# Kernel optimization log

Measured on AMD Instinct MI355X. Metric: run time of the kernel, lower is better.

The kernel has to match this reference:

```python
import jax, jax.numpy as jnp
import numpy as np

H = 12        # num_heads
HD = 64       # head_dim
D = H * HD    # hidden_size = 768
N = 4096      # number of patches (64x64 grid)
SCALE = HD ** -0.5


def _rotate_half(x):
    half = x.shape[-1] // 2
    x1, x2 = x[..., :half], x[..., half:]
    return jnp.concatenate([-x2, x1], axis=-1)


def setup_inputs() -> dict:
    key = jax.random.key(0)
    ks = jax.random.split(key, 7)
    return {
        "hidden_states": jax.random.normal(ks[0], (N, D), jnp.float32),
        "cos": jax.random.uniform(ks[1], (N, HD), jnp.float32),
        "sin": jax.random.uniform(ks[2], (N, HD), jnp.float32),
        "qkv_w": jax.random.normal(ks[3], (D, 3 * D), jnp.float32) * (D ** -0.5),
        "qkv_b": jax.random.normal(ks[4], (3 * D,), jnp.float32) * 0.02,
        "proj_w": jax.random.normal(ks[5], (D, D), jnp.float32) * (D ** -0.5),
        "proj_b": jax.random.normal(ks[6], (D,), jnp.float32) * 0.02,
    }


def reference(hidden_states, cos, sin, qkv_w, qkv_b, proj_w, proj_b):
    n = hidden_states.shape[0]
    # fused QKV projection: (N, 3D) -> (N, 3, H, HD)
    qkv = (hidden_states @ qkv_w + qkv_b).reshape(n, 3, H, HD)
    q, k, v = qkv[:, 0], qkv[:, 1], qkv[:, 2]  # each (N, H, HD)

    # 2-D RoPE (HF apply_rotary_pos_emb_vision): cos/sin broadcast over heads
    c = cos[:, None, :]
    s = sin[:, None, :]
    q = q * c + _rotate_half(q) * s
    k = k * c + _rotate_half(k) * s

    # full bidirectional attention, heads-first layout
    q = q.transpose(1, 0, 2) * SCALE  # (H, N, HD)
    k = k.transpose(1, 0, 2)
    v = v.transpose(1, 0, 2)
    attn = jnp.einsum('hnd,hmd->hnm', q, k)      # (H, N, N)
    attn = jax.nn.softmax(attn, axis=-1)
    out = jnp.einsum('hnm,hmd->hnd', attn, v)    # (H, N, HD)
    out = out.transpose(1, 0, 2).reshape(n, D)
    return out @ proj_w + proj_b
```

## Files before the change

kernel.cpp:

```cpp
#include <hip/hip_runtime.h>
#include <stdint.h>

#define NTOK 4096
#define NH 12
#define HDIM 64
#define DMODEL 768
#define D3 2304

typedef __attribute__((ext_vector_type(8))) __bf16 bf16x8;
typedef __attribute__((ext_vector_type(4))) float f32x4;
typedef __attribute__((ext_vector_type(4))) unsigned int u32x4;

#define MFMA(a, b, c) __builtin_amdgcn_mfma_f32_16x16x32_bf16((a), (b), (c), 0, 0, 0)

__device__ __forceinline__ uint16_t f2bf(float f) {
  uint32_t u = __builtin_bit_cast(uint32_t, f) + 0x8000u;
  return (uint16_t)(u >> 16);
}
__device__ __forceinline__ uint32_t packrd(float a, float b) {
  uint32_t ua = __builtin_bit_cast(uint32_t, a) + 0x8000u;
  uint32_t ub = __builtin_bit_cast(uint32_t, b) + 0x8000u;
  return __builtin_amdgcn_perm(ub, ua, 0x07060302u);
}
__device__ __forceinline__ uint32_t packtr(float a, float b) {
  return __builtin_amdgcn_perm(__builtin_bit_cast(uint32_t, b), __builtin_bit_cast(uint32_t, a),
                               0x07060302u);
}
__device__ __forceinline__ float bf2f(uint16_t u) {
  uint32_t v = ((uint32_t)u) << 16;
  return __builtin_bit_cast(float, v);
}
__device__ __forceinline__ void gld_lds16(const uint16_t* g, uint16_t* l) {
  __builtin_amdgcn_global_load_lds((const __attribute__((address_space(1))) void*)g,
                                   (__attribute__((address_space(3))) void*)l, 16, 0, 0);
}

__global__ void va_cast_bf16(const float* __restrict__ in, uint16_t* __restrict__ out, int n4) {
  int i = blockIdx.x * 256 + threadIdx.x;
  if (i >= n4) return;
  float4 v = ((const float4*)in)[i];
  ((uint2*)out)[i] = make_uint2(packrd(v.x, v.y), packrd(v.z, v.w));
}

__global__ void va_transpose_cast(const float* __restrict__ W, uint16_t* __restrict__ Wt,
                                  int K, int Ncols) {
  __shared__ uint16_t tile[32][36];
  const int t = threadIdx.x;
  const int k0 = blockIdx.y * 32, n0 = blockIdx.x * 32;
  {
    int i = t >> 3, j = (t & 7) * 4;
    float4 v = *(const float4*)(W + (size_t)(k0 + i) * Ncols + n0 + j);
    tile[i][j + 0] = f2bf(v.x);
    tile[i][j + 1] = f2bf(v.y);
    tile[i][j + 2] = f2bf(v.z);
    tile[i][j + 3] = f2bf(v.w);
  }
  __syncthreads();
  {
    int c = t >> 3, kk = (t & 7) * 4;
    uint32_t lo = (uint32_t)tile[kk + 0][c] | ((uint32_t)tile[kk + 1][c] << 16);
    uint32_t hi = (uint32_t)tile[kk + 2][c] | ((uint32_t)tile[kk + 3][c] << 16);
    *(uint2*)(Wt + (size_t)(n0 + c) * K + k0 + kk) = make_uint2(lo, hi);
  }
}

__global__ __launch_bounds__(256) void va_gemm_qkv(const uint16_t* __restrict__ A,
                                                   const uint16_t* __restrict__ Bt,
                                                   const float* __restrict__ bias,
                                                   const float* __restrict__ cosb,
                                                   const float* __restrict__ sinb,
                                                   uint16_t* __restrict__ Qg,
                                                   uint16_t* __restrict__ Kg,
                                                   uint16_t* __restrict__ Vtg) {
  __shared__ uint16_t As[128 * 32];
  __shared__ uint16_t Bs[128 * 32];
  const int t = threadIdx.x;
  const int w = t >> 6, ln = t & 63, quad = ln >> 4, l15 = ln & 15;
  const int m0 = blockIdx.y * 128, n0 = blockIdx.x * 128;
  const int wm = (w & 1) * 64, wn = (w >> 1) * 64;
  const int srow = t >> 2, scol = (t & 3) * 8;
  f32x4 acc[4][4] = {};
  for (int kk = 0; kk < DMODEL; kk += 32) {
#pragma unroll
    for (int p = 0; p < 2; ++p) {
      gld_lds16(A + (size_t)(m0 + p * 64 + srow) * DMODEL + kk + scol,
                As + (p * 64 + w * 16) * 32);
      gld_lds16(Bt + (size_t)(n0 + p * 64 + srow) * DMODEL + kk + scol,
                Bs + (p * 64 + w * 16) * 32);
    }
    __syncthreads();
    bf16x8 af[4], bfr[4];
#pragma unroll
    for (int i = 0; i < 4; ++i) {
      af[i] = *(const bf16x8*)(As + (wm + i * 16 + l15) * 32 + quad * 8);
      bfr[i] = *(const bf16x8*)(Bs + (wn + i * 16 + l15) * 32 + quad * 8);
    }
#pragma unroll
    for (int i = 0; i < 4; ++i)
#pragma unroll
      for (int j = 0; j < 4; ++j) acc[i][j] = MFMA(af[i], bfr[j], acc[i][j]);
    __syncthreads();
  }
  const int col0 = n0 + wn;
  const int type = col0 / DMODEL;
  const int h = (col0 % DMODEL) / HDIM;
  if (type < 2) {
    const float sc = (type == 0) ? (0.125f * 1.4426950408889634f) : 1.0f;
    uint16_t* dst = (type == 0 ? Qg : Kg) + (size_t)h * NTOK * HDIM;
#pragma unroll
    for (int j = 0; j < 2; ++j) {
      const int d = j * 16 + l15, dhi = d + 32;
      const float blo = bias[col0 + d], bhi = bias[col0 + dhi];
#pragma unroll
      for (int i = 0; i < 4; ++i) {
        const int row0 = m0 + wm + i * 16 + quad * 4;
#pragma unroll
        for (int rg = 0; rg < 4; ++rg) {
          const int n = row0 + rg;
          const float a = acc[i][j][rg] + blo;
          const float b = acc[i][j + 2][rg] + bhi;
          const float cl = cosb[(size_t)n * HDIM + d], sl = sinb[(size_t)n * HDIM + d];
          const float ch = cosb[(size_t)n * HDIM + dhi], sh = sinb[(size_t)n * HDIM + dhi];
          *(uint32_t*)(dst + (size_t)n * HDIM + 2 * d) =
              packrd((a * cl - b * sl) * sc, (b * ch + a * sh) * sc);
        }
      }
    }
  } else {
    const int win = (m0 + wm) >> 6;
#pragma unroll
    for (int i = 0; i < 4; ++i) {
      const int H = i & 1, hb = (i >> 1) & 1;
      const int colp = win * 32 + quad * 8 + hb * 4;
#pragma unroll
      for (int j = 0; j < 4; ++j) {
        const int d = j * 16 + l15;
        const float bb = bias[col0 + d];
        uint32_t u0 = packrd(acc[i][j][0] + bb, acc[i][j][1] + bb);
        uint32_t u1 = packrd(acc[i][j][2] + bb, acc[i][j][3] + bb);
        *(uint2*)(Vtg + (((size_t)H * NH + h) * HDIM + d) * 2048 + colp) = make_uint2(u0, u1);
      }
    }
  }
}

__global__ __launch_bounds__(256) void va_gemm_proj(const uint16_t* __restrict__ A,
                                                    const uint16_t* __restrict__ Bt,
                                                    const float* __restrict__ bias,
                                                    float* __restrict__ C, int M, int Nc, int K) {
  __shared__ uint16_t As[64 * 32];
  __shared__ uint16_t Bs[128 * 32];
  const int t = threadIdx.x;
  const int w = t >> 6, ln = t & 63, quad = ln >> 4, l15 = ln & 15;
  const int m0 = blockIdx.y * 64, n0 = blockIdx.x * 128;
  const int wn = w * 32;
  const int srow = t >> 2, scol = (t & 3) * 8;
  f32x4 acc[4][2] = {};
  for (int kk = 0; kk < K; kk += 32) {
    if (srow < 64)
      gld_lds16(A + (size_t)(m0 + srow) * K + kk + scol, As + w * 16 * 32);
#pragma unroll
    for (int p = 0; p < 2; ++p)
      gld_lds16(Bt + (size_t)(n0 + p * 64 + srow) * K + kk + scol, Bs + (p * 64 + w * 16) * 32);
    __syncthreads();
    bf16x8 af[4], bfr[2];
#pragma unroll
    for (int i = 0; i < 4; ++i) af[i] = *(const bf16x8*)(As + (i * 16 + l15) * 32 + quad * 8);
#pragma unroll
    for (int j = 0; j < 2; ++j)
      bfr[j] = *(const bf16x8*)(Bs + (wn + j * 16 + l15) * 32 + quad * 8);
#pragma unroll
    for (int i = 0; i < 4; ++i)
#pragma unroll
      for (int j = 0; j < 2; ++j) acc[i][j] = MFMA(af[i], bfr[j], acc[i][j]);
    __syncthreads();
  }
#pragma unroll
  for (int i = 0; i < 4; ++i) {
    int row = m0 + i * 16 + quad * 4;
#pragma unroll
    for (int j = 0; j < 2; ++j) {
      int col = n0 + wn + j * 16 + l15;
      float b = bias[col];
#pragma unroll
      for (int rg = 0; rg < 4; ++rg) C[(size_t)(row + rg) * Nc + col] = acc[i][j][rg] + b;
    }
  }
}

__global__ __launch_bounds__(256, 3) void va_flash11(const uint16_t* __restrict__ Qg,
                                                     const uint16_t* __restrict__ Kg,
                                                     const uint16_t* __restrict__ Vtg,
                                                     uint16_t* __restrict__ Opb,
                                                     float* __restrict__ Lp) {
  __shared__ uint16_t Ks[2][2][64 * 32];
  __shared__ uint16_t Vs[2][2][64 * 32];
  const int t = threadIdx.x;
  const int w = t >> 6, ln = t & 63, quad = ln >> 4, l15 = ln & 15;
  const int h = blockIdx.y;
  const int qb = blockIdx.x & 31, ks = blockIdx.x >> 5;
  const int q0 = qb * 128, key0 = ks * 2048;

  bf16x8 qf[2][2];
#pragma unroll
  for (int s = 0; s < 2; ++s)
#pragma unroll
    for (int c = 0; c < 2; ++c)
      qf[s][c] = *(const bf16x8*)(Qg + ((size_t)h * NTOK + q0 + w * 32 + s * 16 + l15) * HDIM +
                                  c * 32 + quad * 8);
  const u32x4 onesu = {0x3F803F80u, 0x3F803F80u, 0x3F803F80u, 0x3F803F80u};
  const bf16x8 vones = __builtin_bit_cast(bf16x8, onesu);
  f32x4 o[2][4] = {};
  f32x4 ol[2] = {};
  const uint16_t* Kst =
      Kg + ((size_t)h * NTOK + key0 + w * 16 + (ln >> 2)) * HDIM + (ln & 3) * 8;
  const uint16_t* Vst0 =
      Vtg + (((size_t)0 * NH + h) * HDIM + w * 16 + (ln >> 2)) * 2048 + ks * 1024 + (ln & 3) * 8;
  const uint16_t* Vst1 =
      Vtg + (((size_t)1 * NH + h) * HDIM + w * 16 + (ln >> 2)) * 2048 + ks * 1024 + (ln & 3) * 8;

  gld_lds16(Kst, &Ks[0][0][w * 16 * 32]);
  gld_lds16(Kst + 32, &Ks[0][1][w * 16 * 32]);
  gld_lds16(Vst0, &Vs[0][0][w * 16 * 32]);
  gld_lds16(Vst1, &Vs[0][1][w * 16 * 32]);

  for (int kt = 0; kt < 32; ++kt) {
    __syncthreads();
    const int cur = kt & 1;
    if (kt < 31) {
      Kst += 64 * HDIM;
      Vst0 += 32;
      Vst1 += 32;
      gld_lds16(Kst, &Ks[cur ^ 1][0][w * 16 * 32]);
      gld_lds16(Kst + 32, &Ks[cur ^ 1][1][w * 16 * 32]);
      gld_lds16(Vst0, &Vs[cur ^ 1][0][w * 16 * 32]);
      gld_lds16(Vst1, &Vs[cur ^ 1][1][w * 16 * 32]);
    }
    f32x4 st[2][4];
#pragma unroll
    for (int mt = 0; mt < 4; ++mt) {
      bf16x8 ka0 = *(const bf16x8*)(&Ks[cur][0][(mt * 16 + l15) * 32 + quad * 8]);
      bf16x8 ka1 = *(const bf16x8*)(&Ks[cur][1][(mt * 16 + l15) * 32 + quad * 8]);
#pragma unroll
      for (int s = 0; s < 2; ++s) {
        f32x4 z = {};
        z = MFMA(ka0, qf[s][0], z);
        st[s][mt] = MFMA(ka1, qf[s][1], z);
      }
    }
    bf16x8 vf[4][2];
#pragma unroll
    for (int dt = 0; dt < 4; ++dt)
#pragma unroll
      for (int H = 0; H < 2; ++H)
        vf[dt][H] = *(const bf16x8*)(&Vs[cur][H][(dt * 16 + l15) * 32 + quad * 8]);
#pragma unroll
    for (int s = 0; s < 2; ++s) {
      uint32_t Ppk[4][2];
#pragma unroll
      for (int mt = 0; mt < 4; ++mt) {
        float p0 = __builtin_amdgcn_exp2f(st[s][mt][0]);
        float p1 = __builtin_amdgcn_exp2f(st[s][mt][1]);
        float p2 = __builtin_amdgcn_exp2f(st[s][mt][2]);
        float p3 = __builtin_amdgcn_exp2f(st[s][mt][3]);
        Ppk[mt][0] = packtr(p0, p1);
        Ppk[mt][1] = packtr(p2, p3);
      }
#pragma unroll
      for (int H = 0; H < 2; ++H) {
        u32x4 d = {Ppk[H][0], Ppk[H][1], Ppk[H + 2][0], Ppk[H + 2][1]};
        bf16x8 pf = __builtin_bit_cast(bf16x8, d);
#pragma unroll
        for (int dt = 0; dt < 4; ++dt) o[s][dt] = MFMA(vf[dt][H], pf, o[s][dt]);
        ol[s] = MFMA(vones, pf, ol[s]);
      }
    }
  }
#pragma unroll
  for (int s = 0; s < 2; ++s) {
    const int q = q0 + w * 32 + s * 16 + l15;
    uint16_t* row = Opb + ((size_t)ks * NTOK + q) * DMODEL + h * HDIM + quad * 4;
#pragma unroll
    for (int dt = 0; dt < 4; ++dt) {
      uint32_t u0 = packrd(o[s][dt][0], o[s][dt][1]);
      uint32_t u1 = packrd(o[s][dt][2], o[s][dt][3]);
      *(uint2*)(row + dt * 16) = make_uint2(u0, u1);
    }
    if (quad == 0) Lp[(size_t)(ks * NH + h) * NTOK + q] = ol[s][0];
  }
}

__global__ __launch_bounds__(256) void va_combine2r(const uint16_t* __restrict__ Opb,
                                                    const float* __restrict__ Lp,
                                                    uint16_t* __restrict__ Ob) {
  const int idx = blockIdx.x * 256 + threadIdx.x;
  const int n = idx / 96, c = idx % 96;
  const int h = c >> 3;
  const float inv =
      1.0f / (Lp[(size_t)h * NTOK + n] + Lp[((size_t)NH + h) * NTOK + n]);
  const uint16_t* p0 = Opb + (size_t)n * DMODEL + c * 8;
  const uint16_t* p1 = Opb + ((size_t)NTOK + n) * DMODEL + c * 8;
  uint16_t a[8], b[8];
  *(uint4*)a = *(const uint4*)p0;
  *(uint4*)b = *(const uint4*)p1;
  uint32_t out[4];
#pragma unroll
  for (int j = 0; j < 8; j += 2) {
    float r0 = (bf2f(a[j]) + bf2f(b[j])) * inv;
    float r1 = (bf2f(a[j + 1]) + bf2f(b[j + 1])) * inv;
    out[j >> 1] = packrd(r0, r1);
  }
  *(uint4*)(Ob + (size_t)n * DMODEL + c * 8) = *(uint4*)out;
}

extern "C" void kernel_launch(void* const* d_in, const int* in_sizes, int n_in, void* d_out,
                              int out_size, void* d_ws, size_t ws_size, hipStream_t stream) {
  (void)in_sizes; (void)n_in; (void)out_size; (void)ws_size;
  const float* hidden = (const float*)d_in[0];
  const float* cosb = (const float*)d_in[1];
  const float* sinb = (const float*)d_in[2];
  const float* qkv_w = (const float*)d_in[3];
  const float* qkv_b = (const float*)d_in[4];
  const float* proj_w = (const float*)d_in[5];
  const float* proj_b = (const float*)d_in[6];
  float* out = (float*)d_out;

  char* ws = (char*)d_ws;
  size_t off = 0;
  auto alloc = [&](size_t bytes) {
    void* p = ws + off;
    off += (bytes + 255) & ~(size_t)255;
    return p;
  };
  uint16_t* Abf = (uint16_t*)alloc((size_t)NTOK * DMODEL * 2);
  uint16_t* Wqt = (uint16_t*)alloc((size_t)D3 * DMODEL * 2);
  uint16_t* Wpt = (uint16_t*)alloc((size_t)DMODEL * DMODEL * 2);
  uint16_t* Qb = (uint16_t*)alloc((size_t)NH * NTOK * HDIM * 2);
  uint16_t* Kb = (uint16_t*)alloc((size_t)NH * NTOK * HDIM * 2);
  uint16_t* Vtb = (uint16_t*)alloc((size_t)2 * NH * HDIM * 2048 * 2);
  uint16_t* Ob = (uint16_t*)alloc((size_t)NTOK * DMODEL * 2);
  uint16_t* Opb = (uint16_t*)alloc((size_t)2 * NTOK * DMODEL * 2);
  float* Lp = (float*)alloc((size_t)2 * NH * NTOK * 4);

  va_cast_bf16<<<(NTOK * DMODEL / 4 + 255) / 256, 256, 0, stream>>>(hidden, Abf,
                                                                    NTOK * DMODEL / 4);
  va_transpose_cast<<<dim3(D3 / 32, DMODEL / 32), 256, 0, stream>>>(qkv_w, Wqt, DMODEL, D3);
  va_transpose_cast<<<dim3(DMODEL / 32, DMODEL / 32), 256, 0, stream>>>(proj_w, Wpt, DMODEL,
                                                                        DMODEL);
  va_gemm_qkv<<<dim3(D3 / 128, NTOK / 128), 256, 0, stream>>>(Abf, Wqt, qkv_b, cosb, sinb, Qb,
                                                              Kb, Vtb);
  va_flash11<<<dim3(64, NH), 256, 0, stream>>>(Qb, Kb, Vtb, Opb, Lp);
  va_combine2r<<<(NTOK * DMODEL / 8) / 256, 256, 0, stream>>>(Opb, Lp, Ob);
  va_gemm_proj<<<dim3(DMODEL / 128, NTOK / 64), 256, 0, stream>>>(Ob, Wpt, proj_b, out, NTOK,
                                                                  DMODEL, DMODEL);
}
```

Baseline: 200.0 us.

## Fuse split-KV combine into projection GEMM and pack RoPE cos/sin tables

Removes the separate combine kernel. The projection GEMM now loads the two partial attention outputs and the per-head softmax denominators itself, normalizes them in registers, and writes the bf16 A tile into LDS, with the next tile prefetched. Separately, cos/sin are repacked into interleaved float4s inside the input cast kernel, so the QKV epilogue does one vector load instead of four scalar loads. This saves a launch and the write and re-read of the combined output. The cost is that the combine arithmetic is now repeated for each of the 6 column blocks, and the A operand goes through registers instead of async global-to-LDS loads.

Result: slower. 204.4 us (+2.2%).

```diff
diff --git a/kernel.cpp b/kernel.cpp
--- a/kernel.cpp
+++ b/kernel.cpp
@@ -35,11 +35,20 @@
                                    (__attribute__((address_space(3))) void*)l, 16, 0, 0);
 }
 
-__global__ void va_cast_bf16(const float* __restrict__ in, uint16_t* __restrict__ out, int n4) {
+__global__ void va_cast_cs4(const float* __restrict__ in, uint16_t* __restrict__ out,
+                            const float* __restrict__ cosb, const float* __restrict__ sinb,
+                            float4* __restrict__ cs4, int n4) {
   int i = blockIdx.x * 256 + threadIdx.x;
-  if (i >= n4) return;
-  float4 v = ((const float4*)in)[i];
-  ((uint2*)out)[i] = make_uint2(packrd(v.x, v.y), packrd(v.z, v.w));
+  if (i < n4) {
+    float4 v = ((const float4*)in)[i];
+    ((uint2*)out)[i] = make_uint2(packrd(v.x, v.y), packrd(v.z, v.w));
+    return;
+  }
+  int idx = i - n4;
+  if (idx >= NTOK * 32) return;
+  int n = idx >> 5, d0 = idx & 31;
+  cs4[idx] = make_float4(cosb[n * HDIM + d0], sinb[n * HDIM + d0], cosb[n * HDIM + d0 + 32],
+                         sinb[n * HDIM + d0 + 32]);
 }
 
 __global__ void va_transpose_cast(const float* __restrict__ W, uint16_t* __restrict__ Wt,
@@ -67,8 +76,7 @@
 __global__ __launch_bounds__(256) void va_gemm_qkv(const uint16_t* __restrict__ A,
                                                    const uint16_t* __restrict__ Bt,
                                                    const float* __restrict__ bias,
-                                                   const float* __restrict__ cosb,
-                                                   const float* __restrict__ sinb,
+                                                   const float4* __restrict__ cs4,
                                                    uint16_t* __restrict__ Qg,
                                                    uint16_t* __restrict__ Kg,
                                                    uint16_t* __restrict__ Vtg) {
@@ -109,8 +117,8 @@
     uint16_t* dst = (type == 0 ? Qg : Kg) + (size_t)h * NTOK * HDIM;
 #pragma unroll
     for (int j = 0; j < 2; ++j) {
-      const int d = j * 16 + l15, dhi = d + 32;
-      const float blo = bias[col0 + d], bhi = bias[col0 + dhi];
+      const int d = j * 16 + l15;
+      const float blo = bias[col0 + d], bhi = bias[col0 + d + 32];
 #pragma unroll
       for (int i = 0; i < 4; ++i) {
         const int row0 = m0 + wm + i * 16 + quad * 4;
@@ -119,10 +127,9 @@
           const int n = row0 + rg;
           const float a = acc[i][j][rg] + blo;
           const float b = acc[i][j + 2][rg] + bhi;
-          const float cl = cosb[(size_t)n * HDIM + d], sl = sinb[(size_t)n * HDIM + d];
-          const float ch = cosb[(size_t)n * HDIM + dhi], sh = sinb[(size_t)n * HDIM + dhi];
+          const float4 cs = cs4[n * 32 + d];
           *(uint32_t*)(dst + (size_t)n * HDIM + 2 * d) =
-              packrd((a * cl - b * sl) * sc, (b * ch + a * sh) * sc);
+              packrd((a * cs.x - b * cs.y) * sc, (b * cs.z + a * cs.w) * sc);
         }
       }
     }
@@ -144,10 +151,11 @@
   }
 }
 
-__global__ __launch_bounds__(256) void va_gemm_proj(const uint16_t* __restrict__ A,
+__global__ __launch_bounds__(256) void va_gemm_proj(const uint16_t* __restrict__ Opb,
+                                                    const float* __restrict__ Lp,
                                                     const uint16_t* __restrict__ Bt,
                                                     const float* __restrict__ bias,
-                                                    float* __restrict__ C, int M, int Nc, int K) {
+                                                    float* __restrict__ C) {
   __shared__ uint16_t As[64 * 32];
   __shared__ uint16_t Bs[128 * 32];
   const int t = threadIdx.x;
@@ -155,13 +163,35 @@
   const int m0 = blockIdx.y * 64, n0 = blockIdx.x * 128;
   const int wn = w * 32;
   const int srow = t >> 2, scol = (t & 3) * 8;
+  const int n = m0 + srow;
+  float inv[NH];
+#pragma unroll
+  for (int hh = 0; hh < NH; ++hh)
+    inv[hh] = 1.0f / (Lp[(size_t)hh * NTOK + n] + Lp[((size_t)NH + hh) * NTOK + n]);
+  const uint16_t* pa = Opb + (size_t)n * DMODEL + scol;
+  const uint16_t* pb = pa + (size_t)NTOK * DMODEL;
+  uint16_t ua[8], ub[8];
+  *(uint4*)ua = *(const uint4*)pa;
+  *(uint4*)ub = *(const uint4*)pb;
   f32x4 acc[4][2] = {};
-  for (int kk = 0; kk < K; kk += 32) {
-    if (srow < 64)
-      gld_lds16(A + (size_t)(m0 + srow) * K + kk + scol, As + w * 16 * 32);
+  for (int kk = 0; kk < DMODEL; kk += 32) {
+    {
+      const float iv = inv[(kk + scol) >> 6];
+      uint32_t o[4];
+#pragma unroll
+      for (int j = 0; j < 8; j += 2)
+        o[j >> 1] = packrd((bf2f(ua[j]) + bf2f(ub[j])) * iv,
+                           (bf2f(ua[j + 1]) + bf2f(ub[j + 1])) * iv);
+      *(uint4*)(As + w * 16 * 32 + ln * 8) = *(uint4*)o;
+    }
 #pragma unroll
     for (int p = 0; p < 2; ++p)
-      gld_lds16(Bt + (size_t)(n0 + p * 64 + srow) * K + kk + scol, Bs + (p * 64 + w * 16) * 32);
+      gld_lds16(Bt + (size_t)(n0 + p * 64 + srow) * DMODEL + kk + scol,
+                Bs + (p * 64 + w * 16) * 32);
+    if (kk + 32 < DMODEL) {
+      *(uint4*)ua = *(const uint4*)(pa + kk + 32);
+      *(uint4*)ub = *(const uint4*)(pb + kk + 32);
+    }
     __syncthreads();
     bf16x8 af[4], bfr[2];
 #pragma unroll
@@ -183,7 +213,7 @@
       int col = n0 + wn + j * 16 + l15;
       float b = bias[col];
 #pragma unroll
-      for (int rg = 0; rg < 4; ++rg) C[(size_t)(row + rg) * Nc + col] = acc[i][j][rg] + b;
+      for (int rg = 0; rg < 4; ++rg) C[(size_t)(row + rg) * DMODEL + col] = acc[i][j][rg] + b;
     }
   }
 }
@@ -290,29 +320,6 @@
   }
 }
 
-__global__ __launch_bounds__(256) void va_combine2r(const uint16_t* __restrict__ Opb,
-                                                    const float* __restrict__ Lp,
-                                                    uint16_t* __restrict__ Ob) {
-  const int idx = blockIdx.x * 256 + threadIdx.x;
-  const int n = idx / 96, c = idx % 96;
-  const int h = c >> 3;
-  const float inv =
-      1.0f / (Lp[(size_t)h * NTOK + n] + Lp[((size_t)NH + h) * NTOK + n]);
-  const uint16_t* p0 = Opb + (size_t)n * DMODEL + c * 8;
-  const uint16_t* p1 = Opb + ((size_t)NTOK + n) * DMODEL + c * 8;
-  uint16_t a[8], b[8];
-  *(uint4*)a = *(const uint4*)p0;
-  *(uint4*)b = *(const uint4*)p1;
-  uint32_t out[4];
-#pragma unroll
-  for (int j = 0; j < 8; j += 2) {
-    float r0 = (bf2f(a[j]) + bf2f(b[j])) * inv;
-    float r1 = (bf2f(a[j + 1]) + bf2f(b[j + 1])) * inv;
-    out[j >> 1] = packrd(r0, r1);
-  }
-  *(uint4*)(Ob + (size_t)n * DMODEL + c * 8) = *(uint4*)out;
-}
-
 extern "C" void kernel_launch(void* const* d_in, const int* in_sizes, int n_in, void* d_out,
                               int out_size, void* d_ws, size_t ws_size, hipStream_t stream) {
   (void)in_sizes; (void)n_in; (void)out_size; (void)ws_size;
@@ -335,22 +342,21 @@
   uint16_t* Abf = (uint16_t*)alloc((size_t)NTOK * DMODEL * 2);
   uint16_t* Wqt = (uint16_t*)alloc((size_t)D3 * DMODEL * 2);
   uint16_t* Wpt = (uint16_t*)alloc((size_t)DMODEL * DMODEL * 2);
+  float4* cs4 = (float4*)alloc((size_t)NTOK * 32 * 16);
   uint16_t* Qb = (uint16_t*)alloc((size_t)NH * NTOK * HDIM * 2);
   uint16_t* Kb = (uint16_t*)alloc((size_t)NH * NTOK * HDIM * 2);
   uint16_t* Vtb = (uint16_t*)alloc((size_t)2 * NH * HDIM * 2048 * 2);
-  uint16_t* Ob = (uint16_t*)alloc((size_t)NTOK * DMODEL * 2);
   uint16_t* Opb = (uint16_t*)alloc((size_t)2 * NTOK * DMODEL * 2);
   float* Lp = (float*)alloc((size_t)2 * NH * NTOK * 4);
 
-  va_cast_bf16<<<(NTOK * DMODEL / 4 + 255) / 256, 256, 0, stream>>>(hidden, Abf,
-                                                                    NTOK * DMODEL / 4);
+  const int n4 = NTOK * DMODEL / 4;
+  va_cast_cs4<<<(n4 + NTOK * 32 + 255) / 256, 256, 0, stream>>>(hidden, Abf, cosb, sinb, cs4,
+                                                                n4);
   va_transpose_cast<<<dim3(D3 / 32, DMODEL / 32), 256, 0, stream>>>(qkv_w, Wqt, DMODEL, D3);
   va_transpose_cast<<<dim3(DMODEL / 32, DMODEL / 32), 256, 0, stream>>>(proj_w, Wpt, DMODEL,
                                                                         DMODEL);
-  va_gemm_qkv<<<dim3(D3 / 128, NTOK / 128), 256, 0, stream>>>(Abf, Wqt, qkv_b, cosb, sinb, Qb,
-                                                              Kb, Vtb);
+  va_gemm_qkv<<<dim3(D3 / 128, NTOK / 128), 256, 0, stream>>>(Abf, Wqt, qkv_b, cs4, Qb, Kb,
+                                                              Vtb);
   va_flash11<<<dim3(64, NH), 256, 0, stream>>>(Qb, Kb, Vtb, Opb, Lp);
-  va_combine2r<<<(NTOK * DMODEL / 8) / 256, 256, 0, stream>>>(Opb, Lp, Ob);
-  va_gemm_proj<<<dim3(DMODEL / 128, NTOK / 64), 256, 0, stream>>>(Ob, Wpt, proj_b, out, NTOK,
-                                                                  DMODEL, DMODEL);
-}
+  va_gemm_proj<<<dim3(DMODEL / 128, NTOK / 64), 256, 0, stream>>>(Opb, Lp, Wpt, proj_b, out);
+}
```
